# Kernel optimization log

Measured on AMD Instinct MI355X. Metric: run time of the kernel, lower is better.

The kernel has to match this reference:

```python
import jax, jax.numpy as jnp
import numpy as np
from jax import lax


def setup_inputs() -> dict:
    key = jax.random.key(0)
    ks = jax.random.split(key, 6)
    B = 65536
    x = jax.random.normal(ks[0], (B, 784), dtype=jnp.float32)
    conv_w = jax.random.normal(ks[1], (3, 3), dtype=jnp.float32)
    w1 = jax.random.normal(ks[2], (676, 128), dtype=jnp.float32) * 0.05
    b1 = jax.random.normal(ks[3], (128,), dtype=jnp.float32) * 0.05
    w2 = jax.random.normal(ks[4], (128, 10), dtype=jnp.float32) * 0.05
    b2 = jax.random.normal(ks[5], (10,), dtype=jnp.float32) * 0.05
    return {"x": x, "conv_w": conv_w, "w1": w1, "b1": b1, "w2": w2, "b2": b2}


def reference(x, conv_w, w1, b1, w2, b2):
    B = x.shape[0]
    img = x.reshape(B, 1, 28, 28)  # NCHW
    # valid 3x3 cross-correlation (tensordot over patch == cross-correlation)
    conv = lax.conv_general_dilated(
        img, conv_w[None, None], window_strides=(1, 1), padding="VALID",
        dimension_numbers=("NCHW", "OIHW", "NCHW"))  # [B,1,26,26]
    h = conv.reshape(B, 26 * 26)
    h = jax.nn.relu(h @ w1 + b1)
    return h @ w2 + b2
```

## Files before the change

### kernel.cpp

```cpp
#include <hip/hip_runtime.h>

typedef __attribute__((ext_vector_type(4))) float floatx4;
typedef __attribute__((ext_vector_type(8))) short short8;
typedef __attribute__((ext_vector_type(8))) unsigned short ushort8v;

__device__ __forceinline__ unsigned short f2bf(float f) {
  unsigned int u = __builtin_bit_cast(unsigned int, f);
  u += 0x7FFFu + ((u >> 16) & 1u);
  return (unsigned short)(u >> 16);
}

#define KTOT 784
#define KP   800
#define N1   128
#define BM   128
#define LDH  132

typedef const __attribute__((address_space(1))) unsigned int* gas_ptr;
typedef __attribute__((address_space(3))) unsigned int* las_ptr;
__device__ __forceinline__ void dma16(const float* g, float* l) {
  __builtin_amdgcn_global_load_lds((gas_ptr)g, (las_ptr)l, 16, 0, 0);
}

__global__ void prep_w1eff(const float* __restrict__ conv_w,
                           const float* __restrict__ w1,
                           unsigned short* __restrict__ Bt) {
  const int n = blockIdx.x;
  float cw[9];
#pragma unroll
  for (int i = 0; i < 9; ++i) cw[i] = conv_w[i];
  for (int q = threadIdx.x; q < KP; q += blockDim.x) {
    float acc = 0.f;
    if (q < KTOT) {
      const int r = q / 28, c = q % 28;
#pragma unroll
      for (int di = 0; di < 3; ++di) {
        const int i2 = r - di;
        if (i2 < 0 || i2 >= 26) continue;
#pragma unroll
        for (int dj = 0; dj < 3; ++dj) {
          const int j2 = c - dj;
          if (j2 < 0 || j2 >= 26) continue;
          acc += cw[di * 3 + dj] * w1[(i2 * 26 + j2) * N1 + n];
        }
      }
    }
    Bt[n * KP + q] = f2bf(acc);
  }
}

__global__ __launch_bounds__(512, 4)
void fused_mlp(const float* __restrict__ x,
               const unsigned short* __restrict__ Bt,
               const float* __restrict__ b1,
               const float* __restrict__ w2,
               const float* __restrict__ b2,
               float* __restrict__ out) {
  __shared__ __align__(16) unsigned char smem[38592];
  float* sAf = (float*)smem;
  unsigned short* sH = (unsigned short*)smem;
  unsigned short* sW2t = (unsigned short*)(smem + 33792);
  float* sB1 = (float*)(smem + 38016);
  float* sB2 = (float*)(smem + 38528);

  const int tid  = threadIdx.x;
  const int wave = tid >> 6;
  const int lane = tid & 63;
  const int wm = wave >> 1;
  const int wn = wave & 1;
  const int lr = lane & 15;
  const int lq = lane >> 4;

  const long row_base = (long)blockIdx.x * BM;
  const float* xblk = x + row_base * KTOT;

  for (int i = tid; i < 16 * N1; i += 512) {
    const int n = i >> 7, k = i & 127;
    sW2t[n * LDH + k] = (n < 10) ? f2bf(w2[k * 10 + n]) : (unsigned short)0;
  }
  if (tid < N1) sB1[tid] = b1[tid];
  if (tid >= N1 && tid < N1 + 10) sB2[tid - N1] = b2[tid - N1];

  const int i0 = wave * 2, i1 = wave * 2 + 1;
  const int rsub = lane >> 3;
  const int cg = (lane & 7) ^ (rsub & 6);
  const int ceff = (cg < 4) ? cg : cg - 4;
  const float* gA0 = xblk + (long)(i0 * 8 + rsub) * KTOT + cg * 4;
  const float* gA1 = xblk + (long)(i1 * 8 + rsub) * KTOT + cg * 4;
  const float* gT0 = xblk + (long)(i0 * 8 + rsub) * KTOT + 768 + ceff * 4;
  const float* gT1 = xblk + (long)(i1 * 8 + rsub) * KTOT + 768 + ceff * 4;

  const unsigned short* bptr[4];
#pragma unroll
  for (int in = 0; in < 4; ++in)
    bptr[in] = Bt + (long)(wn * 64 + in * 16 + lr) * KP + lq * 8;

  floatx4 acc[2][4] = {};

  dma16(gA0, sAf + i0 * 256);
  dma16(gA1, sAf + i1 * 256);

  for (int kt = 0; kt < 25; ++kt) {
    const int buf = kt & 1;
    ushort8v rB[4];
#pragma unroll
    for (int in = 0; in < 4; ++in)
      rB[in] = *(const ushort8v*)(bptr[in] + kt * 32);
    asm volatile("s_waitcnt vmcnt(4)\n\ts_barrier" ::: "memory");
    {
      const int d = (kt + 1 <= 24) ? kt + 1 : 24;
      const float* g0 = (d < 24) ? gA0 + d * 32 : gT0;
      const float* g1 = (d < 24) ? gA1 + d * 32 : gT1;
      float* ldst = sAf + (buf ^ 1) * 4096;
      dma16(g0, ldst + i0 * 256);
      dma16(g1, ldst + i1 * 256);
    }
    const float* A = sAf + buf * 4096;
    short8 af[2];
#pragma unroll
    for (int im = 0; im < 2; ++im) {
      const int r = wm * 32 + im * 16 + lr;
      const int s0 = (2 * lq) ^ (r & 6);
      const floatx4* p = (const floatx4*)(A + r * 32 + s0 * 4);
      const floatx4 q0 = p[0], q1 = p[1];
      ushort8v u;
#pragma unroll
      for (int j = 0; j < 4; ++j) { u[j] = f2bf(q0[j]); u[4 + j] = f2bf(q1[j]); }
      af[im] = __builtin_bit_cast(short8, u);
    }
#pragma unroll
    for (int im = 0; im < 2; ++im)
#pragma unroll
      for (int in = 0; in < 4; ++in)
        acc[im][in] = __builtin_amdgcn_mfma_f32_16x16x32_bf16(
            af[im], __builtin_bit_cast(short8, rB[in]), acc[im][in], 0, 0, 0);
  }

  __syncthreads();

#pragma unroll
  for (int im = 0; im < 2; ++im) {
#pragma unroll
    for (int in = 0; in < 4; ++in) {
      const int col = wn * 64 + in * 16 + lr;
      const float bb = sB1[col];
#pragma unroll
      for (int r = 0; r < 4; ++r) {
        const int row = wm * 32 + im * 16 + lq * 4 + r;
        const float v = acc[im][in][r] + bb;
        sH[row * LDH + col] = f2bf(v > 0.f ? v : 0.f);
      }
    }
  }
  __syncthreads();

  floatx4 o = {0.f, 0.f, 0.f, 0.f};
  const int m0 = wave * 16;
#pragma unroll
  for (int kc = 0; kc < 4; ++kc) {
    const int kof = kc * 32 + lq * 8;
    const short8 wv = *(const short8*)&sW2t[lr * LDH + kof];
    const short8 a0 = *(const short8*)&sH[(m0 + lr) * LDH + kof];
    o = __builtin_amdgcn_mfma_f32_16x16x32_bf16(a0, wv, o, 0, 0, 0);
  }
  if (lr < 10) {
    const float bb = sB2[lr];
#pragma unroll
    for (int r = 0; r < 4; ++r) {
      const long row = row_base + m0 + lq * 4 + r;
      out[row * 10 + lr] = o[r] + bb;
    }
  }
}

extern "C" void kernel_launch(void* const* d_in, const int* in_sizes, int n_in,
                              void* d_out, int out_size, void* d_ws, size_t ws_size,
                              hipStream_t stream) {
  const float* x      = (const float*)d_in[0];
  const float* conv_w = (const float*)d_in[1];
  const float* w1     = (const float*)d_in[2];
  const float* b1     = (const float*)d_in[3];
  const float* w2     = (const float*)d_in[4];
  const float* b2     = (const float*)d_in[5];
  float* out = (float*)d_out;

  unsigned short* Bt = (unsigned short*)d_ws;

  prep_w1eff<<<128, 256, 0, stream>>>(conv_w, w1, Bt);
  fused_mlp<<<65536 / BM, 512, 0, stream>>>(x, Bt, b1, w2, b2, out);
}
```

Measured before the change: 306.9 us.

## Replace double-buffered A prefetch with synchronous 64-column K stages

The rolling double-buffered global-to-LDS prefetch is replaced by a loop of 12 stages plus a tail. Each stage loads 64 columns of x into both LDS buffers, synchronizes, then runs two MFMA substeps. The padded weight width grows to 832 so the last stage can read zero-padded weights for the duplicated tail columns. The aim is to halve the number of barrier rounds per K sweep. In exchange the code gives up overlap between loads and MFMA within a block and relies on other resident blocks to hide load latency.

```diff
diff --git a/kernel.cpp b/kernel.cpp
--- a/kernel.cpp
+++ b/kernel.cpp
@@ -11,7 +11,7 @@
 }
 
 #define KTOT 784
-#define KP   800
+#define KP2  832
 #define N1   128
 #define BM   128
 #define LDH  132
@@ -29,7 +29,7 @@
   float cw[9];
 #pragma unroll
   for (int i = 0; i < 9; ++i) cw[i] = conv_w[i];
-  for (int q = threadIdx.x; q < KP; q += blockDim.x) {
+  for (int q = threadIdx.x; q < KP2; q += blockDim.x) {
     float acc = 0.f;
     if (q < KTOT) {
       const int r = q / 28, c = q % 28;
@@ -45,7 +45,7 @@
         }
       }
     }
-    Bt[n * KP + q] = f2bf(acc);
+    Bt[n * KP2 + q] = f2bf(acc);
   }
 }
 
@@ -81,59 +81,73 @@
   if (tid < N1) sB1[tid] = b1[tid];
   if (tid >= N1 && tid < N1 + 10) sB2[tid - N1] = b2[tid - N1];
 
-  const int i0 = wave * 2, i1 = wave * 2 + 1;
   const int rsub = lane >> 3;
-  const int cg = (lane & 7) ^ (rsub & 6);
+  const int cg   = (lane & 7) ^ (rsub & 6);
   const int ceff = (cg < 4) ? cg : cg - 4;
-  const float* gA0 = xblk + (long)(i0 * 8 + rsub) * KTOT + cg * 4;
-  const float* gA1 = xblk + (long)(i1 * 8 + rsub) * KTOT + cg * 4;
-  const float* gT0 = xblk + (long)(i0 * 8 + rsub) * KTOT + 768 + ceff * 4;
-  const float* gT1 = xblk + (long)(i1 * 8 + rsub) * KTOT + 768 + ceff * 4;
+  const int r0 = wave * 16 + rsub;
+  const int r1 = wave * 16 + 8 + rsub;
+  const float* g0 = xblk + (long)r0 * KTOT + cg * 4;
+  const float* g1 = xblk + (long)r1 * KTOT + cg * 4;
+  float* l00 = sAf + (wave * 2) * 256;
+  float* l01 = sAf + (wave * 2 + 1) * 256;
+  float* l10 = sAf + 4096 + (wave * 2) * 256;
+  float* l11 = sAf + 4096 + (wave * 2 + 1) * 256;
 
   const unsigned short* bptr[4];
 #pragma unroll
   for (int in = 0; in < 4; ++in)
-    bptr[in] = Bt + (long)(wn * 64 + in * 16 + lr) * KP + lq * 8;
+    bptr[in] = Bt + (long)(wn * 64 + in * 16 + lr) * KP2 + lq * 8;
 
   floatx4 acc[2][4] = {};
 
-  dma16(gA0, sAf + i0 * 256);
-  dma16(gA1, sAf + i1 * 256);
-
-  for (int kt = 0; kt < 25; ++kt) {
-    const int buf = kt & 1;
-    ushort8v rB[4];
-#pragma unroll
-    for (int in = 0; in < 4; ++in)
-      rB[in] = *(const ushort8v*)(bptr[in] + kt * 32);
-    asm volatile("s_waitcnt vmcnt(4)\n\ts_barrier" ::: "memory");
-    {
-      const int d = (kt + 1 <= 24) ? kt + 1 : 24;
-      const float* g0 = (d < 24) ? gA0 + d * 32 : gT0;
-      const float* g1 = (d < 24) ? gA1 + d * 32 : gT1;
-      float* ldst = sAf + (buf ^ 1) * 4096;
-      dma16(g0, ldst + i0 * 256);
-      dma16(g1, ldst + i1 * 256);
-    }
-    const float* A = sAf + buf * 4096;
-    short8 af[2];
-#pragma unroll
-    for (int im = 0; im < 2; ++im) {
-      const int r = wm * 32 + im * 16 + lr;
-      const int s0 = (2 * lq) ^ (r & 6);
-      const floatx4* p = (const floatx4*)(A + r * 32 + s0 * 4);
-      const floatx4 q0 = p[0], q1 = p[1];
-      ushort8v u;
-#pragma unroll
-      for (int j = 0; j < 4; ++j) { u[j] = f2bf(q0[j]); u[4 + j] = f2bf(q1[j]); }
-      af[im] = __builtin_bit_cast(short8, u);
-    }
-#pragma unroll
-    for (int im = 0; im < 2; ++im)
+  auto compute_step = [&](int kt) {
+#pragma unroll
+    for (int s = 0; s < 2; ++s) {
+      ushort8v rB[4];
 #pragma unroll
       for (int in = 0; in < 4; ++in)
-        acc[im][in] = __builtin_amdgcn_mfma_f32_16x16x32_bf16(
-            af[im], __builtin_bit_cast(short8, rB[in]), acc[im][in], 0, 0, 0);
+        rB[in] = *(const ushort8v*)(bptr[in] + kt * 64 + s * 32);
+      short8 af[2];
+#pragma unroll
+      for (int im = 0; im < 2; ++im) {
+        const int r = wm * 32 + im * 16 + lr;
+        const int s0 = (2 * lq) ^ (r & 6);
+        const floatx4* p = (const floatx4*)(sAf + s * 4096 + r * 32 + s0 * 4);
+        const floatx4 q0 = p[0], q1 = p[1];
+        ushort8v u;
+#pragma unroll
+        for (int j = 0; j < 4; ++j) { u[j] = f2bf(q0[j]); u[4 + j] = f2bf(q1[j]); }
+        af[im] = __builtin_bit_cast(short8, u);
+      }
+#pragma unroll
+      for (int im = 0; im < 2; ++im)
+#pragma unroll
+        for (int in = 0; in < 4; ++in)
+          acc[im][in] = __builtin_amdgcn_mfma_f32_16x16x32_bf16(
+              af[im], __builtin_bit_cast(short8, rB[in]), acc[im][in], 0, 0, 0);
+    }
+  };
+
+  for (int kt = 0; kt < 12; ++kt) {
+    const int ko = kt * 64;
+    __syncthreads();
+    dma16(g0 + ko,      l00);
+    dma16(g1 + ko,      l01);
+    dma16(g0 + ko + 32, l10);
+    dma16(g1 + ko + 32, l11);
+    __syncthreads();
+    compute_step(kt);
+  }
+  {
+    const float* t0 = xblk + (long)r0 * KTOT + 768 + ceff * 4;
+    const float* t1 = xblk + (long)r1 * KTOT + 768 + ceff * 4;
+    __syncthreads();
+    dma16(t0, l00);
+    dma16(t1, l01);
+    dma16(t0, l10);
+    dma16(t1, l11);
+    __syncthreads();
+    compute_step(12);
   }
 
   __syncthreads();
```

New measurement: 325.8 us. 6.1% more time.
